# Kernel tuning notes

Measured on AMD Instinct MI355X. Metric: run time of the kernel, lower is better.

## Reference

```python
import jax, jax.numpy as jnp
import numpy as np

N_NODES = 100000
N_EDGES = 3200000
EMB_DIM = 128


def setup_inputs() -> dict:
    key = jax.random.key(0)
    k_emb, k_w1, k_w2, k_e = jax.random.split(key, 4)
    emb = jax.random.normal(k_emb, (N_NODES, EMB_DIM), dtype=jnp.float32)
    W1 = jax.random.normal(k_w1, (EMB_DIM, 64), dtype=jnp.float32) * (1.0 / np.sqrt(EMB_DIM))
    b1 = jnp.zeros((64,), dtype=jnp.float32)
    W2 = jax.random.normal(k_w2, (64, 32), dtype=jnp.float32) * (1.0 / np.sqrt(64))
    b2 = jnp.zeros((32,), dtype=jnp.float32)
    edge_index = jax.random.randint(k_e, (2, N_EDGES), 0, N_NODES, dtype=jnp.int64)
    return {"embedding": emb, "W1": W1, "b1": b1, "W2": W2, "b2": b2,
            "edge_index": edge_index}


def gcn_conv(x, W, b, src, dst, n):
    # PyG GCNConv defaults: add self-loops, symmetric normalization D^-1/2 (A+I) D^-1/2,
    # linear transform first, then gather-scale-scatter aggregation, then bias.
    xw = x @ W                                                  # [N, out]
    ones = jnp.ones(src.shape, dtype=xw.dtype)
    deg = jax.ops.segment_sum(ones, dst, num_segments=n) + 1.0  # in-degree + self-loop
    dis = jax.lax.rsqrt(deg)                                    # deg >= 1 always
    norm = dis[src] * dis[dst]                                  # [E]
    agg = jax.ops.segment_sum(xw[src] * norm[:, None], dst, num_segments=n)
    agg = agg + (dis * dis)[:, None] * xw                       # self-loop messages
    return agg + b


def reference(embedding, W1, b1, W2, b2, edge_index):
    n = embedding.shape[0]
    src, dst = edge_index[0], edge_index[1]
    # encode
    h = jax.nn.relu(gcn_conv(embedding, W1, b1, src, dst, n))
    z = gcn_conv(h, W2, b2, src, dst, n)                        # [N, 32]
    # decode: per-edge gather-dot-sigmoid
    logits = jnp.sum(z[src] * z[dst], axis=1)                   # [E]
    return jax.nn.sigmoid(logits)
```

## Files before the change

### kernel.cpp

```cpp
#include <hip/hip_runtime.h>
#include <hip/hip_bf16.h>
#include <math.h>

#define NN 100000
#define NE 3200000
#define NPAD 100096
#define NB 392
#define BN 256
#define EPB 4096
#define NBLK 782
#define SLOT 9728

typedef __attribute__((ext_vector_type(8))) short short8;
typedef __attribute__((ext_vector_type(4))) float floatx4;
typedef __attribute__((ext_vector_type(4))) unsigned uint4v;

__device__ __forceinline__ unsigned short bf16_of(float x) {
    __hip_bfloat16 h = __float2bfloat16(x);
    return *(unsigned short*)&h;
}
__device__ __forceinline__ unsigned pack2(float a, float b) {
    return (unsigned)bf16_of(a) | ((unsigned)bf16_of(b) << 16);
}
__device__ __forceinline__ float lo_f(unsigned u) { return __uint_as_float(u << 16); }
__device__ __forceinline__ float hi_f(unsigned u) { return __uint_as_float(u & 0xffff0000u); }
__device__ __forceinline__ void acc8(float* a, uint4v r) {
    a[0] += lo_f(r[0]); a[1] += hi_f(r[0]);
    a[2] += lo_f(r[1]); a[3] += hi_f(r[1]);
    a[4] += lo_f(r[2]); a[5] += hi_f(r[2]);
    a[6] += lo_f(r[3]); a[7] += hi_f(r[3]);
}

__global__ __launch_bounds__(512) void scatter_kernel(const int* __restrict__ src,
                                                      const int* __restrict__ dst,
                                                      int* __restrict__ gcur,
                                                      int* __restrict__ staged) {
    __shared__ int cnt[NB];
    __shared__ int lbase[NB + 1];
    __shared__ int gbase[NB];
    __shared__ int sbuf[EPB];
    __shared__ unsigned short sbkt[EPB];
    int t = threadIdx.x;
    for (int i = t; i < NB; i += 512) cnt[i] = 0;
    __syncthreads();
    int e0 = blockIdx.x * EPB;
    int e1 = min(e0 + EPB, NE);
    int cn = e1 - e0;
    for (int e = e0 + t; e < e1; e += 512) atomicAdd(&cnt[dst[e] >> 8], 1);
    __syncthreads();
    if (t < 64) {
        int v[7]; int s = 0;
#pragma unroll
        for (int k = 0; k < 7; ++k) { int idx = t * 7 + k; v[k] = (idx < NB) ? cnt[idx] : 0; s += v[k]; }
        int inc = s;
#pragma unroll
        for (int m = 1; m < 64; m <<= 1) {
            int u = __shfl_up(inc, m, 64);
            if (t >= m) inc += u;
        }
        int run = inc - s;
#pragma unroll
        for (int k = 0; k < 7; ++k) { int idx = t * 7 + k; if (idx < NB) lbase[idx] = run; run += v[k]; }
        if (t == 63) lbase[NB] = inc;
    }
    __syncthreads();
    for (int i = t; i < NB; i += 512) {
        int c = cnt[i];
        gbase[i] = i * SLOT + atomicAdd(&gcur[i], c);
        cnt[i] = lbase[i];
    }
    __syncthreads();
    for (int e = e0 + t; e < e1; e += 512) {
        int s = src[e], d = dst[e];
        int bk = d >> 8;
        int r = atomicAdd(&cnt[bk], 1);
        sbuf[r] = (s << 8) | (d & (BN - 1));
        sbkt[r] = (unsigned short)bk;
    }
    __syncthreads();
    for (int i = t; i < cn; i += 512) {
        int bk = sbkt[i];
        staged[gbase[bk] + i - lbase[bk]] = sbuf[i];
    }
}

__global__ __launch_bounds__(1024) void fine_kernel(const int* __restrict__ staged,
                                                    const int* __restrict__ gcur,
                                                    int2* __restrict__ offs2,
                                                    float* __restrict__ dis,
                                                    int* __restrict__ csr_src) {
    __shared__ int hist[BN];
    __shared__ int offs[BN];
    __shared__ int cur[BN];
    int t = threadIdx.x, j = blockIdx.x;
    int bb = j * SLOT;
    int be = bb + gcur[j];
    for (int i = t; i < BN; i += 1024) hist[i] = 0;
    __syncthreads();
    for (int e = bb + t; e < be; e += 1024) atomicAdd(&hist[staged[e] & (BN - 1)], 1);
    __syncthreads();
    if (t < 64) {
        int v[4]; int s = 0;
#pragma unroll
        for (int k = 0; k < 4; ++k) { v[k] = hist[t * 4 + k]; s += v[k]; }
        int inc = s;
#pragma unroll
        for (int m = 1; m < 64; m <<= 1) {
            int u = __shfl_up(inc, m, 64);
            if (t >= m) inc += u;
        }
        int run = inc - s;
#pragma unroll
        for (int k = 0; k < 4; ++k) { offs[t * 4 + k] = run; run += v[k]; }
    }
    __syncthreads();
    for (int l = t; l < BN; l += 1024) {
        cur[l] = offs[l];
        int n = j * BN + l;
        if (n < NN) {
            int st = bb + offs[l];
            offs2[n] = make_int2(st, st + hist[l]);
            dis[n] = rsqrtf((float)hist[l] + 1.0f);
        }
    }
    __syncthreads();
    for (int e = bb + t; e < be; e += 1024) {
        int p = staged[e];
        int r = atomicAdd(&cur[p & (BN - 1)], 1);
        csr_src[bb + r] = p >> 8;
    }
}

__global__ __launch_bounds__(256) void mm1_kernel(const float* __restrict__ x,
                                                  const float* __restrict__ W,
                                                  const float* __restrict__ dis,
                                                  unsigned short* __restrict__ y) {
    __shared__ unsigned short Wt[64][136];
    int t = threadIdx.x;
    for (int i = t; i < 128 * 64; i += 256) {
        int k = i >> 6, n = i & 63;
        Wt[n][k] = bf16_of(W[i]);
    }
    __syncthreads();
    int wave = t >> 6, lane = t & 63;
    int quad = lane >> 4, n16 = lane & 15;
    short8 bfr[4][4];
#pragma unroll
    for (int s = 0; s < 4; ++s)
#pragma unroll
        for (int tt = 0; tt < 4; ++tt)
            bfr[s][tt] = *(const short8*)&Wt[tt * 16 + n16][s * 32 + quad * 8];
    int tile0 = (blockIdx.x * 4 + wave) * 4;
#pragma unroll 1
    for (int it = 0; it < 4; ++it) {
        int tile = tile0 + it;
        if (tile >= 6250) break;
        int m0 = tile * 16;
        const float* xp = x + (size_t)(m0 + n16) * 128 + quad * 8;
        floatx4 acc0 = {0,0,0,0}, acc1 = {0,0,0,0}, acc2 = {0,0,0,0}, acc3 = {0,0,0,0};
#pragma unroll
        for (int s = 0; s < 4; ++s) {
            float4 lo = *(const float4*)(xp + s * 32);
            float4 hi = *(const float4*)(xp + s * 32 + 4);
            short8 a;
            a[0] = (short)bf16_of(lo.x); a[1] = (short)bf16_of(lo.y);
            a[2] = (short)bf16_of(lo.z); a[3] = (short)bf16_of(lo.w);
            a[4] = (short)bf16_of(hi.x); a[5] = (short)bf16_of(hi.y);
            a[6] = (short)bf16_of(hi.z); a[7] = (short)bf16_of(hi.w);
            acc0 = __builtin_amdgcn_mfma_f32_16x16x32_bf16(a, bfr[s][0], acc0, 0, 0, 0);
            acc1 = __builtin_amdgcn_mfma_f32_16x16x32_bf16(a, bfr[s][1], acc1, 0, 0, 0);
            acc2 = __builtin_amdgcn_mfma_f32_16x16x32_bf16(a, bfr[s][2], acc2, 0, 0, 0);
            acc3 = __builtin_amdgcn_mfma_f32_16x16x32_bf16(a, bfr[s][3], acc3, 0, 0, 0);
        }
#pragma unroll
        for (int r = 0; r < 4; ++r) {
            int ro = m0 + quad * 4 + r;
            float sc = dis[ro];
            unsigned short* yp = y + (size_t)ro * 64 + n16;
            yp[0]  = bf16_of(acc0[r] * sc);
            yp[16] = bf16_of(acc1[r] * sc);
            yp[32] = bf16_of(acc2[r] * sc);
            yp[48] = bf16_of(acc3[r] * sc);
        }
    }
}

__global__ __launch_bounds__(256) void agg64mm2_kernel(const uint4v* __restrict__ ys4,
                                                       const float* __restrict__ dis,
                                                       const int2* __restrict__ offs2,
                                                       const int* __restrict__ csr_src,
                                                       const float* __restrict__ b1,
                                                       const float* __restrict__ W2,
                                                       unsigned int* __restrict__ ys2) {
    __shared__ float w2s[64 * 32];
    __shared__ float hbuf[32 * 68];
    int t = threadIdx.x;
    for (int i = t; i < 2048; i += 256) w2s[i] = W2[i];
    __syncthreads();
    int tid = blockIdx.x * 256 + t;
    int nd = tid >> 3, c = tid & 7;
    int2 se = offs2[nd];
    int start = se.x, end = se.y;
    float acc[8] = {0, 0, 0, 0, 0, 0, 0, 0};
    acc8(acc, ys4[(size_t)nd * 8 + c]);
    int i = start;
    int n8 = start + ((end - start) & ~7);
    for (; i < n8; i += 8) {
        int s0 = csr_src[i],     s1 = csr_src[i + 1], s2 = csr_src[i + 2], s3 = csr_src[i + 3];
        int s4 = csr_src[i + 4], s5 = csr_src[i + 5], s6 = csr_src[i + 6], s7 = csr_src[i + 7];
        uint4v r0 = ys4[(size_t)s0 * 8 + c];
        uint4v r1 = ys4[(size_t)s1 * 8 + c];
        uint4v r2 = ys4[(size_t)s2 * 8 + c];
        uint4v r3 = ys4[(size_t)s3 * 8 + c];
        uint4v r4 = ys4[(size_t)s4 * 8 + c];
        uint4v r5 = ys4[(size_t)s5 * 8 + c];
        uint4v r6 = ys4[(size_t)s6 * 8 + c];
        uint4v r7 = ys4[(size_t)s7 * 8 + c];
        acc8(acc, r0); acc8(acc, r1); acc8(acc, r2); acc8(acc, r3);
        acc8(acc, r4); acc8(acc, r5); acc8(acc, r6); acc8(acc, r7);
    }
    for (; i < end; ++i) acc8(acc, ys4[(size_t)csr_src[i] * 8 + c]);
    float ds = dis[nd];
    const float4 bv0 = *(const float4*)&b1[c * 8];
    const float4 bv1 = *(const float4*)&b1[c * 8 + 4];
    float* hrow = &hbuf[(t >> 3) * 68];
    float4 h0, h1;
    h0.x = fmaxf(fmaf(ds, acc[0], bv0.x), 0.f);
    h0.y = fmaxf(fmaf(ds, acc[1], bv0.y), 0.f);
    h0.z = fmaxf(fmaf(ds, acc[2], bv0.z), 0.f);
    h0.w = fmaxf(fmaf(ds, acc[3], bv0.w), 0.f);
    h1.x = fmaxf(fmaf(ds, acc[4], bv1.x), 0.f);
    h1.y = fmaxf(fmaf(ds, acc[5], bv1.y), 0.f);
    h1.z = fmaxf(fmaf(ds, acc[6], bv1.z), 0.f);
    h1.w = fmaxf(fmaf(ds, acc[7], bv1.w), 0.f);
    *(float4*)&hrow[c * 8]     = h0;
    *(float4*)&hrow[c * 8 + 4] = h1;
    float p0 = 0.f, p1 = 0.f, p2 = 0.f, p3 = 0.f;
#pragma unroll 8
    for (int k = 0; k < 64; ++k) {
        float hk = hrow[k];
        const float4 wr = *(const float4*)&w2s[k * 32 + c * 4];
        p0 = fmaf(hk, wr.x, p0);
        p1 = fmaf(hk, wr.y, p1);
        p2 = fmaf(hk, wr.z, p2);
        p3 = fmaf(hk, wr.w, p3);
    }
    p0 *= ds; p1 *= ds; p2 *= ds; p3 *= ds;
    unsigned int* zp = ys2 + (size_t)nd * 16 + c * 2;
    zp[0] = pack2(p0, p1);
    zp[1] = pack2(p2, p3);
}

__global__ __launch_bounds__(256) void agg32_kernel(const uint4v* __restrict__ ys4,
                                                    const float* __restrict__ dis,
                                                    const int2* __restrict__ offs2,
                                                    const int* __restrict__ csr_src,
                                                    const float* __restrict__ b,
                                                    uint4v* __restrict__ z4) {
    int tid = blockIdx.x * 256 + threadIdx.x;
    int nd = tid >> 2, c = tid & 3;
    if (nd >= NN) return;
    int2 se = offs2[nd];
    int start = se.x, end = se.y;
    float acc[8] = {0, 0, 0, 0, 0, 0, 0, 0};
    acc8(acc, ys4[(size_t)nd * 4 + c]);
    int i = start;
    int n8 = start + ((end - start) & ~7);
    for (; i < n8; i += 8) {
        int s0 = csr_src[i],     s1 = csr_src[i + 1], s2 = csr_src[i + 2], s3 = csr_src[i + 3];
        int s4 = csr_src[i + 4], s5 = csr_src[i + 5], s6 = csr_src[i + 6], s7 = csr_src[i + 7];
        uint4v r0 = ys4[(size_t)s0 * 4 + c];
        uint4v r1 = ys4[(size_t)s1 * 4 + c];
        uint4v r2 = ys4[(size_t)s2 * 4 + c];
        uint4v r3 = ys4[(size_t)s3 * 4 + c];
        uint4v r4 = ys4[(size_t)s4 * 4 + c];
        uint4v r5 = ys4[(size_t)s5 * 4 + c];
        uint4v r6 = ys4[(size_t)s6 * 4 + c];
        uint4v r7 = ys4[(size_t)s7 * 4 + c];
        acc8(acc, r0); acc8(acc, r1); acc8(acc, r2); acc8(acc, r3);
        acc8(acc, r4); acc8(acc, r5); acc8(acc, r6); acc8(acc, r7);
    }
    for (; i < end; ++i) acc8(acc, ys4[(size_t)csr_src[i] * 4 + c]);
    float ds = dis[nd];
    const float4 bv0 = *(const float4*)&b[c * 8];
    const float4 bv1 = *(const float4*)&b[c * 8 + 4];
    uint4v o;
    o[0] = pack2(fmaf(ds, acc[0], bv0.x), fmaf(ds, acc[1], bv0.y));
    o[1] = pack2(fmaf(ds, acc[2], bv0.z), fmaf(ds, acc[3], bv0.w));
    o[2] = pack2(fmaf(ds, acc[4], bv1.x), fmaf(ds, acc[5], bv1.y));
    o[3] = pack2(fmaf(ds, acc[6], bv1.z), fmaf(ds, acc[7], bv1.w));
    z4[(size_t)nd * 4 + c] = o;
}

__global__ __launch_bounds__(256) void decode_kernel(const uint4v* __restrict__ z4,
                                                     const int* __restrict__ src,
                                                     const int* __restrict__ dst,
                                                     float* __restrict__ out) {
    int tid = blockIdx.x * 256 + threadIdx.x;
    int e = tid >> 2, k = tid & 3;
    if (e >= NE) return;
    int s = src[e], d = dst[e];
    uint4v ra = z4[(size_t)s * 4 + k];
    uint4v rb = z4[(size_t)d * 4 + k];
    float acc;
    acc  = lo_f(ra[0]) * lo_f(rb[0]) + hi_f(ra[0]) * hi_f(rb[0]);
    acc += lo_f(ra[1]) * lo_f(rb[1]) + hi_f(ra[1]) * hi_f(rb[1]);
    acc += lo_f(ra[2]) * lo_f(rb[2]) + hi_f(ra[2]) * hi_f(rb[2]);
    acc += lo_f(ra[3]) * lo_f(rb[3]) + hi_f(ra[3]) * hi_f(rb[3]);
#pragma unroll
    for (int m = 2; m >= 1; m >>= 1) acc += __shfl_xor(acc, m, 4);
    if (k == 0) out[e] = 1.0f / (1.0f + expf(-acc));
}

extern "C" void kernel_launch(void* const* d_in, const int* in_sizes, int n_in,
                              void* d_out, int out_size, void* d_ws, size_t ws_size,
                              hipStream_t stream) {
    const float* emb = (const float*)d_in[0];
    const float* W1  = (const float*)d_in[1];
    const float* b1  = (const float*)d_in[2];
    const float* W2  = (const float*)d_in[3];
    const float* b2  = (const float*)d_in[4];
    const int*   ei  = (const int*)d_in[5];
    const int* src = ei;
    const int* dst = ei + NE;
    float* out = (float*)d_out;

    char* w = (char*)d_ws;
    int2*  offs2       = (int2*)w;          w += (size_t)NPAD * 8;
    float* dis         = (float*)w;         w += (size_t)NPAD * 4;
    int*   gcur        = (int*)w;           w += 2048;
    int*   csr_src     = (int*)w;           w += (size_t)NB * SLOT * 4;
    int*   staged      = (int*)w;           w += (size_t)NB * SLOT * 4;
    unsigned short* ysbuf = (unsigned short*)w; w += (size_t)NN * 64 * 2;
    unsigned short* ys2 = (unsigned short*)w;
    unsigned short* ys1 = ysbuf;
    unsigned short* z   = ysbuf;

    hipMemsetAsync(gcur, 0, NB * 4, stream);
    scatter_kernel<<<NBLK, 512, 0, stream>>>(src, dst, gcur, staged);
    fine_kernel<<<NB, 1024, 0, stream>>>(staged, gcur, offs2, dis, csr_src);

    mm1_kernel<<<391, 256, 0, stream>>>(emb, W1, dis, ys1);
    agg64mm2_kernel<<<(NN * 8) / 256, 256, 0, stream>>>((const uint4v*)ys1, dis, offs2, csr_src,
                                                        b1, W2, (unsigned int*)ys2);
    agg32_kernel<<<(NN * 4 + 255) / 256, 256, 0, stream>>>((const uint4v*)ys2, dis, offs2, csr_src, b2, (uint4v*)z);

    decode_kernel<<<(NE * 4) / 256, 256, 0, stream>>>((const uint4v*)z, src, dst, out);
}
```

Before: 325.7 us.

## Fuse first matmul into scatter kernel and move source scaling into aggregation

The X·W1 matmul no longer depends on degrees. It now runs in extra blocks of the edge-scatter launch, so it overlaps with CSR construction and one launch is removed. The per-source D^-1/2 scaling moves into the layer-1 aggregation, which now gathers dis[src] for every edge. This adds roughly 3.2M scattered 4-byte loads to the gather loop and shares LDS through a union.

```diff
diff --git a/kernel.cpp b/kernel.cpp
--- a/kernel.cpp
+++ b/kernel.cpp
@@ -10,6 +10,7 @@
 #define EPB 4096
 #define NBLK 782
 #define SLOT 9728
+#define MMBLK 391
 
 typedef __attribute__((ext_vector_type(8))) short short8;
 typedef __attribute__((ext_vector_type(4))) float floatx4;
@@ -30,57 +31,119 @@
     a[4] += lo_f(r[2]); a[5] += hi_f(r[2]);
     a[6] += lo_f(r[3]); a[7] += hi_f(r[3]);
 }
-
-__global__ __launch_bounds__(512) void scatter_kernel(const int* __restrict__ src,
-                                                      const int* __restrict__ dst,
-                                                      int* __restrict__ gcur,
-                                                      int* __restrict__ staged) {
-    __shared__ int cnt[NB];
-    __shared__ int lbase[NB + 1];
-    __shared__ int gbase[NB];
-    __shared__ int sbuf[EPB];
-    __shared__ unsigned short sbkt[EPB];
+__device__ __forceinline__ void acc8s(float* a, uint4v r, float d) {
+    a[0] = fmaf(lo_f(r[0]), d, a[0]); a[1] = fmaf(hi_f(r[0]), d, a[1]);
+    a[2] = fmaf(lo_f(r[1]), d, a[2]); a[3] = fmaf(hi_f(r[1]), d, a[3]);
+    a[4] = fmaf(lo_f(r[2]), d, a[4]); a[5] = fmaf(hi_f(r[2]), d, a[5]);
+    a[6] = fmaf(lo_f(r[3]), d, a[6]); a[7] = fmaf(hi_f(r[3]), d, a[7]);
+}
+
+__global__ __launch_bounds__(512) void scatter_mm1_kernel(const int* __restrict__ src,
+                                                          const int* __restrict__ dst,
+                                                          int* __restrict__ gcur,
+                                                          int* __restrict__ staged,
+                                                          const float* __restrict__ x,
+                                                          const float* __restrict__ W1,
+                                                          unsigned short* __restrict__ y) {
+    __shared__ union {
+        struct {
+            int cnt[NB];
+            int lbase[NB + 1];
+            int gbase[NB];
+            int sbuf[EPB];
+            unsigned short sbkt[EPB];
+        } sc;
+        unsigned short Wt[64][136];
+    } sm;
     int t = threadIdx.x;
-    for (int i = t; i < NB; i += 512) cnt[i] = 0;
-    __syncthreads();
-    int e0 = blockIdx.x * EPB;
-    int e1 = min(e0 + EPB, NE);
-    int cn = e1 - e0;
-    for (int e = e0 + t; e < e1; e += 512) atomicAdd(&cnt[dst[e] >> 8], 1);
-    __syncthreads();
-    if (t < 64) {
-        int v[7]; int s = 0;
-#pragma unroll
-        for (int k = 0; k < 7; ++k) { int idx = t * 7 + k; v[k] = (idx < NB) ? cnt[idx] : 0; s += v[k]; }
-        int inc = s;
-#pragma unroll
-        for (int m = 1; m < 64; m <<= 1) {
-            int u = __shfl_up(inc, m, 64);
-            if (t >= m) inc += u;
-        }
-        int run = inc - s;
-#pragma unroll
-        for (int k = 0; k < 7; ++k) { int idx = t * 7 + k; if (idx < NB) lbase[idx] = run; run += v[k]; }
-        if (t == 63) lbase[NB] = inc;
-    }
-    __syncthreads();
-    for (int i = t; i < NB; i += 512) {
-        int c = cnt[i];
-        gbase[i] = i * SLOT + atomicAdd(&gcur[i], c);
-        cnt[i] = lbase[i];
-    }
-    __syncthreads();
-    for (int e = e0 + t; e < e1; e += 512) {
-        int s = src[e], d = dst[e];
-        int bk = d >> 8;
-        int r = atomicAdd(&cnt[bk], 1);
-        sbuf[r] = (s << 8) | (d & (BN - 1));
-        sbkt[r] = (unsigned short)bk;
-    }
-    __syncthreads();
-    for (int i = t; i < cn; i += 512) {
-        int bk = sbkt[i];
-        staged[gbase[bk] + i - lbase[bk]] = sbuf[i];
+    if (blockIdx.x < NBLK) {
+        for (int i = t; i < NB; i += 512) sm.sc.cnt[i] = 0;
+        __syncthreads();
+        int e0 = blockIdx.x * EPB;
+        int e1 = min(e0 + EPB, NE);
+        int cn = e1 - e0;
+        for (int e = e0 + t; e < e1; e += 512) atomicAdd(&sm.sc.cnt[dst[e] >> 8], 1);
+        __syncthreads();
+        if (t < 64) {
+            int v[7]; int s = 0;
+#pragma unroll
+            for (int k = 0; k < 7; ++k) { int idx = t * 7 + k; v[k] = (idx < NB) ? sm.sc.cnt[idx] : 0; s += v[k]; }
+            int inc = s;
+#pragma unroll
+            for (int m = 1; m < 64; m <<= 1) {
+                int u = __shfl_up(inc, m, 64);
+                if (t >= m) inc += u;
+            }
+            int run = inc - s;
+#pragma unroll
+            for (int k = 0; k < 7; ++k) { int idx = t * 7 + k; if (idx < NB) sm.sc.lbase[idx] = run; run += v[k]; }
+            if (t == 63) sm.sc.lbase[NB] = inc;
+        }
+        __syncthreads();
+        for (int i = t; i < NB; i += 512) {
+            int c = sm.sc.cnt[i];
+            sm.sc.gbase[i] = i * SLOT + atomicAdd(&gcur[i], c);
+            sm.sc.cnt[i] = sm.sc.lbase[i];
+        }
+        __syncthreads();
+        for (int e = e0 + t; e < e1; e += 512) {
+            int s = src[e], d = dst[e];
+            int bk = d >> 8;
+            int r = atomicAdd(&sm.sc.cnt[bk], 1);
+            sm.sc.sbuf[r] = (s << 8) | (d & (BN - 1));
+            sm.sc.sbkt[r] = (unsigned short)bk;
+        }
+        __syncthreads();
+        for (int i = t; i < cn; i += 512) {
+            int bk = sm.sc.sbkt[i];
+            staged[sm.sc.gbase[bk] + i - sm.sc.lbase[bk]] = sm.sc.sbuf[i];
+        }
+    } else {
+        for (int i = t; i < 128 * 64; i += 512) {
+            int k = i >> 6, n = i & 63;
+            sm.Wt[n][k] = bf16_of(W1[i]);
+        }
+        __syncthreads();
+        int wave = t >> 6, lane = t & 63;
+        int quad = lane >> 4, n16 = lane & 15;
+        short8 bfr[4][4];
+#pragma unroll
+        for (int s = 0; s < 4; ++s)
+#pragma unroll
+            for (int tt = 0; tt < 4; ++tt)
+                bfr[s][tt] = *(const short8*)&sm.Wt[tt * 16 + n16][s * 32 + quad * 8];
+        int tile0 = ((blockIdx.x - NBLK) * 8 + wave) * 2;
+#pragma unroll 1
+        for (int it = 0; it < 2; ++it) {
+            int tile = tile0 + it;
+            if (tile >= 6250) break;
+            int m0 = tile * 16;
+            const float* xp = x + (size_t)(m0 + n16) * 128 + quad * 8;
+            floatx4 acc0 = {0,0,0,0}, acc1 = {0,0,0,0}, acc2 = {0,0,0,0}, acc3 = {0,0,0,0};
+#pragma unroll
+            for (int s = 0; s < 4; ++s) {
+                float4 lo = *(const float4*)(xp + s * 32);
+                float4 hi = *(const float4*)(xp + s * 32 + 4);
+                short8 a;
+                a[0] = (short)bf16_of(lo.x); a[1] = (short)bf16_of(lo.y);
+                a[2] = (short)bf16_of(lo.z); a[3] = (short)bf16_of(lo.w);
+                a[4] = (short)bf16_of(hi.x); a[5] = (short)bf16_of(hi.y);
+                a[6] = (short)bf16_of(hi.z); a[7] = (short)bf16_of(hi.w);
+                acc0 = __builtin_amdgcn_mfma_f32_16x16x32_bf16(a, bfr[s][0], acc0, 0, 0, 0);
+                acc1 = __builtin_amdgcn_mfma_f32_16x16x32_bf16(a, bfr[s][1], acc1, 0, 0, 0);
+                acc2 = __builtin_amdgcn_mfma_f32_16x16x32_bf16(a, bfr[s][2], acc2, 0, 0, 0);
+                acc3 = __builtin_amdgcn_mfma_f32_16x16x32_bf16(a, bfr[s][3], acc3, 0, 0, 0);
+            }
+#pragma unroll
+            for (int r = 0; r < 4; ++r) {
+                int ro = m0 + quad * 4 + r;
+                unsigned short* yp = y + (size_t)ro * 64 + n16;
+                yp[0]  = bf16_of(acc0[r]);
+                yp[16] = bf16_of(acc1[r]);
+                yp[32] = bf16_of(acc2[r]);
+                yp[48] = bf16_of(acc3[r]);
+            }
+        }
     }
 }
 
@@ -131,60 +194,6 @@
     }
 }
 
-__global__ __launch_bounds__(256) void mm1_kernel(const float* __restrict__ x,
-                                                  const float* __restrict__ W,
-                                                  const float* __restrict__ dis,
-                                                  unsigned short* __restrict__ y) {
-    __shared__ unsigned short Wt[64][136];
-    int t = threadIdx.x;
-    for (int i = t; i < 128 * 64; i += 256) {
-        int k = i >> 6, n = i & 63;
-        Wt[n][k] = bf16_of(W[i]);
-    }
-    __syncthreads();
-    int wave = t >> 6, lane = t & 63;
-    int quad = lane >> 4, n16 = lane & 15;
-    short8 bfr[4][4];
-#pragma unroll
-    for (int s = 0; s < 4; ++s)
-#pragma unroll
-        for (int tt = 0; tt < 4; ++tt)
-            bfr[s][tt] = *(const short8*)&Wt[tt * 16 + n16][s * 32 + quad * 8];
-    int tile0 = (blockIdx.x * 4 + wave) * 4;
-#pragma unroll 1
-    for (int it = 0; it < 4; ++it) {
-        int tile = tile0 + it;
-        if (tile >= 6250) break;
-        int m0 = tile * 16;
-        const float* xp = x + (size_t)(m0 + n16) * 128 + quad * 8;
-        floatx4 acc0 = {0,0,0,0}, acc1 = {0,0,0,0}, acc2 = {0,0,0,0}, acc3 = {0,0,0,0};
-#pragma unroll
-        for (int s = 0; s < 4; ++s) {
-            float4 lo = *(const float4*)(xp + s * 32);
-            float4 hi = *(const float4*)(xp + s * 32 + 4);
-            short8 a;
-            a[0] = (short)bf16_of(lo.x); a[1] = (short)bf16_of(lo.y);
-            a[2] = (short)bf16_of(lo.z); a[3] = (short)bf16_of(lo.w);
-            a[4] = (short)bf16_of(hi.x); a[5] = (short)bf16_of(hi.y);
-            a[6] = (short)bf16_of(hi.z); a[7] = (short)bf16_of(hi.w);
-            acc0 = __builtin_amdgcn_mfma_f32_16x16x32_bf16(a, bfr[s][0], acc0, 0, 0, 0);
-            acc1 = __builtin_amdgcn_mfma_f32_16x16x32_bf16(a, bfr[s][1], acc1, 0, 0, 0);
-            acc2 = __builtin_amdgcn_mfma_f32_16x16x32_bf16(a, bfr[s][2], acc2, 0, 0, 0);
-            acc3 = __builtin_amdgcn_mfma_f32_16x16x32_bf16(a, bfr[s][3], acc3, 0, 0, 0);
-        }
-#pragma unroll
-        for (int r = 0; r < 4; ++r) {
-            int ro = m0 + quad * 4 + r;
-            float sc = dis[ro];
-            unsigned short* yp = y + (size_t)ro * 64 + n16;
-            yp[0]  = bf16_of(acc0[r] * sc);
-            yp[16] = bf16_of(acc1[r] * sc);
-            yp[32] = bf16_of(acc2[r] * sc);
-            yp[48] = bf16_of(acc3[r] * sc);
-        }
-    }
-}
-
 __global__ __launch_bounds__(256) void agg64mm2_kernel(const uint4v* __restrict__ ys4,
                                                        const float* __restrict__ dis,
                                                        const int2* __restrict__ offs2,
@@ -202,12 +211,15 @@
     int2 se = offs2[nd];
     int start = se.x, end = se.y;
     float acc[8] = {0, 0, 0, 0, 0, 0, 0, 0};
-    acc8(acc, ys4[(size_t)nd * 8 + c]);
+    float dnd = dis[nd];
+    acc8s(acc, ys4[(size_t)nd * 8 + c], dnd);
     int i = start;
     int n8 = start + ((end - start) & ~7);
     for (; i < n8; i += 8) {
         int s0 = csr_src[i],     s1 = csr_src[i + 1], s2 = csr_src[i + 2], s3 = csr_src[i + 3];
         int s4 = csr_src[i + 4], s5 = csr_src[i + 5], s6 = csr_src[i + 6], s7 = csr_src[i + 7];
+        float d0 = dis[s0], d1 = dis[s1], d2 = dis[s2], d3 = dis[s3];
+        float d4 = dis[s4], d5 = dis[s5], d6 = dis[s6], d7 = dis[s7];
         uint4v r0 = ys4[(size_t)s0 * 8 + c];
         uint4v r1 = ys4[(size_t)s1 * 8 + c];
         uint4v r2 = ys4[(size_t)s2 * 8 + c];
@@ -216,11 +228,14 @@
         uint4v r5 = ys4[(size_t)s5 * 8 + c];
         uint4v r6 = ys4[(size_t)s6 * 8 + c];
         uint4v r7 = ys4[(size_t)s7 * 8 + c];
-        acc8(acc, r0); acc8(acc, r1); acc8(acc, r2); acc8(acc, r3);
-        acc8(acc, r4); acc8(acc, r5); acc8(acc, r6); acc8(acc, r7);
-    }
-    for (; i < end; ++i) acc8(acc, ys4[(size_t)csr_src[i] * 8 + c]);
-    float ds = dis[nd];
+        acc8s(acc, r0, d0); acc8s(acc, r1, d1); acc8s(acc, r2, d2); acc8s(acc, r3, d3);
+        acc8s(acc, r4, d4); acc8s(acc, r5, d5); acc8s(acc, r6, d6); acc8s(acc, r7, d7);
+    }
+    for (; i < end; ++i) {
+        int s = csr_src[i];
+        acc8s(acc, ys4[(size_t)s * 8 + c], dis[s]);
+    }
+    float ds = dnd;
     const float4 bv0 = *(const float4*)&b1[c * 8];
     const float4 bv1 = *(const float4*)&b1[c * 8 + 4];
     float* hrow = &hbuf[(t >> 3) * 68];
@@ -337,10 +352,9 @@
     unsigned short* z   = ysbuf;
 
     hipMemsetAsync(gcur, 0, NB * 4, stream);
-    scatter_kernel<<<NBLK, 512, 0, stream>>>(src, dst, gcur, staged);
+    scatter_mm1_kernel<<<NBLK + MMBLK, 512, 0, stream>>>(src, dst, gcur, staged, emb, W1, ys1);
     fine_kernel<<<NB, 1024, 0, stream>>>(staged, gcur, offs2, dis, csr_src);
 
-    mm1_kernel<<<391, 256, 0, stream>>>(emb, W1, dis, ys1);
     agg64mm2_kernel<<<(NN * 8) / 256, 256, 0, stream>>>((const uint4v*)ys1, dis, offs2, csr_src,
                                                         b1, W2, (unsigned int*)ys2);
     agg32_kernel<<<(NN * 4 + 255) / 256, 256, 0, stream>>>((const uint4v*)ys2, dis, offs2, csr_src, b2, (uint4v*)z);
```

Result: no change. 323.2 us (-0.8%).
